# Kernel optimization log

Measured on AMD Instinct MI355X. Metric: run time of the kernel, lower is better.

Reference implementation:

```python
import jax, jax.numpy as jnp
from jax import lax
import numpy as np

BS, C_IN, C_OUT, STYLE_D, H, W, F = 8, 256, 256, 512, 64, 64, 3


def setup_inputs() -> dict:
    key = jax.random.key(0)
    k = jax.random.split(key, 6)
    # xavier_uniform for conv weight: gain=1, fan_in=c_in*f*f, fan_out=c_out*f*f
    fan_in, fan_out = C_IN * F * F, C_OUT * F * F
    limit_w = float(np.sqrt(6.0 / (fan_in + fan_out)))
    limit_a = float(np.sqrt(1.0 / STYLE_D))  # torch Linear default init bound
    return {
        "x": jax.random.normal(k[0], (BS, C_IN, H, W), jnp.float32),
        "s": jax.random.normal(k[1], (BS, STYLE_D), jnp.float32),
        "w": jax.random.uniform(k[2], (C_OUT, C_IN, F, F), jnp.float32, -limit_w, limit_w),
        "b": jnp.zeros((C_OUT, 1, 1), jnp.float32),
        "affine_w": jax.random.uniform(k[3], (C_IN, STYLE_D), jnp.float32, -limit_a, limit_a),
        "affine_b": jax.random.uniform(k[4], (C_IN,), jnp.float32, -limit_a, limit_a),
    }


def reference(x, s, w, b, affine_w, affine_b):
    bs = x.shape[0]
    # style -> per-channel modulation scales: [bs, c_in]
    style = s @ affine_w.T + affine_b
    # modulate: [bs, c_out, c_in, f, f]
    wmod = w[None, :, :, :, :] * (style[:, None, :, None, None] + 1.0)
    # demodulate
    d = jnp.sqrt(jnp.sum(jnp.square(wmod), axis=(2, 3, 4), keepdims=True) + 1e-8)
    wmod = wmod / d
    # grouped conv with groups=bs (per-sample weights)
    xr = x.reshape(1, bs * x.shape[1], x.shape[2], x.shape[3])
    cw = wmod.reshape(bs * wmod.shape[1], wmod.shape[2], wmod.shape[3], wmod.shape[4])
    out = lax.conv_general_dilated(
        xr, cw, window_strides=(1, 1), padding=((1, 1), (1, 1)),
        dimension_numbers=("NCHW", "OIHW", "NCHW"), feature_group_count=bs)
    out = out.reshape(bs, wmod.shape[1], out.shape[2], out.shape[3])
    return out + b  # b broadcasts as [c_out,1,1]
```

## Files before the change

kernel.cpp:

```cpp
#include <hip/hip_runtime.h>
#include <hip/hip_bf16.h>
#include <stdint.h>

#define BS   8
#define CIN  256
#define COUT 256
#define SD   512
#define HH   64
#define WW   64
#define HP   66

typedef __attribute__((ext_vector_type(8))) short short8;
typedef __attribute__((ext_vector_type(4))) float f32x4;

__device__ __forceinline__ unsigned short f2bf(float f) {
    __hip_bfloat16 h = __float2bfloat16(f);
    return *reinterpret_cast<unsigned short*>(&h);
}

typedef __attribute__((address_space(3))) unsigned int lds_u32_t;
typedef const __attribute__((address_space(1))) unsigned int glb_u32_t;

__device__ __forceinline__ void async16(const void* g, void* l) {
    __builtin_amdgcn_global_load_lds((glb_u32_t*)g, (lds_u32_t*)l, 16, 0, 0);
}

__global__ void k_style(const float* __restrict__ s, const float* __restrict__ aw,
                        const float* __restrict__ ab, float* __restrict__ m) {
    int b = blockIdx.x >> 3, chunk = blockIdx.x & 7;
    int tid = threadIdx.x;
    __shared__ float sv[SD];
    for (int d = tid; d < SD; d += 256) sv[d] = s[b * SD + d];
    __syncthreads();
    int il = tid >> 3, p = tid & 7;
    int i = chunk * 32 + il;
    const float4* awr = (const float4*)(aw + (size_t)i * SD + p * 64);
    float acc = 0.f;
#pragma unroll
    for (int d4 = 0; d4 < 16; ++d4) {
        float4 w4 = awr[d4];
        int d0 = p * 64 + d4 * 4;
        acc += w4.x * sv[d0] + w4.y * sv[d0 + 1] + w4.z * sv[d0 + 2] + w4.w * sv[d0 + 3];
    }
    acc += __shfl_xor(acc, 1);
    acc += __shfl_xor(acc, 2);
    acc += __shfl_xor(acc, 4);
    if (p == 0) m[b * CIN + i] = acc + ab[i] + 1.0f;
}

__global__ void k_prep(const float* __restrict__ w, const float* __restrict__ m,
                       const float* __restrict__ x,
                       unsigned short* __restrict__ wb, float* __restrict__ dinv,
                       unsigned short* __restrict__ xp) {
    __shared__ float red[4][8];
    int tid = threadIdx.x;

    if (blockIdx.x < COUT) {
        int o = blockIdx.x, i = tid;
        const float* wp = w + ((size_t)o * CIN + i) * 9;
        float v[9];
        float q = 0.f;
#pragma unroll
        for (int t = 0; t < 9; ++t) { v[t] = wp[t]; q += v[t] * v[t]; }
#pragma unroll
        for (int t = 0; t < 9; ++t)
            wb[((size_t)t * COUT + o) * CIN + i] = f2bf(v[t]);

        float r[8];
#pragma unroll
        for (int b = 0; b < 8; ++b) {
            float mv = m[b * CIN + i];
            r[b] = q * mv * mv;
        }
#pragma unroll
        for (int b = 0; b < 8; ++b) {
            r[b] += __shfl_xor(r[b], 1);
            r[b] += __shfl_xor(r[b], 2);
            r[b] += __shfl_xor(r[b], 4);
            r[b] += __shfl_xor(r[b], 8);
            r[b] += __shfl_xor(r[b], 16);
            r[b] += __shfl_xor(r[b], 32);
        }
        int lane = i & 63, wid = i >> 6;
        if (lane == 0) {
#pragma unroll
            for (int b = 0; b < 8; ++b) red[wid][b] = r[b];
        }
        __syncthreads();
        if (i < 8) {
            float acc = red[0][i] + red[1][i] + red[2][i] + red[3][i];
            dinv[i * COUT + o] = rsqrtf(acc + 1e-8f);
        }
        return;
    }

    int bi = blockIdx.x - COUT;
    int b = bi / HP, yp = bi % HP;
    unsigned short* row = xp + ((size_t)(b * HP + yp)) * HP * CIN;

    if (yp == 0 || yp == HP - 1) {
        uint4 z = {0u, 0u, 0u, 0u};
        uint4* r = (uint4*)row;
        for (int j = tid; j < HP * CIN / 8; j += 256) r[j] = z;
        return;
    }
    int y = yp - 1;

    if (tid < 64) {
        uint4 z = {0u, 0u, 0u, 0u};
        if (tid < 32) ((uint4*)row)[tid] = z;
        else ((uint4*)(row + (size_t)(HP - 1) * CIN))[tid - 32] = z;
    }

#pragma unroll
    for (int it = 0; it < 2; ++it) {
        int u = it * 256 + tid;
        int x0 = (u & 15) * 4;
        int i0 = (u >> 4) * 8;
        float vv[8][4];
        float mv[8];
#pragma unroll
        for (int k = 0; k < 8; ++k) {
            *(float4*)vv[k] = *(const float4*)&x[(((size_t)b * CIN + i0 + k) * HH + y) * WW + x0];
            mv[k] = m[b * CIN + i0 + k];
        }
#pragma unroll
        for (int j = 0; j < 4; ++j) {
            short8 p;
#pragma unroll
            for (int k = 0; k < 8; ++k)
                p[k] = (short)f2bf(vv[k][j] * mv[k]);
            *(short8*)&row[(size_t)(x0 + j + 1) * CIN + i0] = p;
        }
    }
}

__global__ void __launch_bounds__(256, 2)
k_conv(const unsigned short* __restrict__ xp,
       const unsigned short* __restrict__ wb,
       const float* __restrict__ dinv,
       const float* __restrict__ bias,
       float* __restrict__ out) {
    __shared__ unsigned short Ar[3168 * 8];
    __shared__ unsigned short Bs[3 * 512 * 8];

    int bx = blockIdx.x;
    int mt = bx & 127;
    int n0 = (bx >> 7) << 6;
    int m0 = mt << 8;
    int b  = m0 >> 12;
    int y0 = (m0 >> 6) & 63;

    int tid = threadIdx.x;
    int lane = tid & 63, w = tid >> 6;
    int quad = lane >> 4, mrow = lane & 15;

    f32x4 acc[4][4] = {};

    const unsigned short* xb = xp + (size_t)b * HP * HP * CIN;

    auto stageA = [&](int kc) {
        int ch0 = kc * 64;
#pragma unroll
        for (int k = 0; k < 12; ++k) {
            int sA = k * 256 + tid;
            int rowA = sA / 528;
            int rem = sA - rowA * 528;
            int colA = rem >> 3, c4 = rem & 7;
            async16(xb + ((size_t)(y0 + rowA) * HP + colA) * CIN + ch0 + ((c4 ^ (colA & 7)) << 3),
                    &Ar[sA * 8]);
        }
        if (tid < 96) {
            int sA = 3072 + tid;
            int rowA = sA / 528;
            int rem = sA - rowA * 528;
            int colA = rem >> 3, c4 = rem & 7;
            async16(xb + ((size_t)(y0 + rowA) * HP + colA) * CIN + ch0 + ((c4 ^ (colA & 7)) << 3),
                    &Ar[sA * 8]);
        }
    };

    auto stageB = [&](int tt, int kcc, int buf) {
        const unsigned short* bp = wb + ((size_t)tt * COUT + n0) * CIN + kcc * 64;
        unsigned short* dst = Bs + buf * 4096;
#pragma unroll
        for (int k = 0; k < 2; ++k) {
            int sB = k * 256 + tid;
            int rowB = sB >> 3, c4 = sB & 7;
            async16(bp + (size_t)rowB * CIN + ((c4 ^ (rowB & 7)) << 3), dst + sB * 8);
        }
    };

    stageA(0);
    stageB(0, 0, 0);
    stageB(1, 0, 1);
    __syncthreads();

#pragma unroll 1
    for (int kc = 0; kc < 4; ++kc) {
#pragma unroll
        for (int t = 0; t < 9; ++t) {
            if (t < 7) stageB(t + 2, kc, (t + 2) % 3);
            else if (kc < 3) stageB(t - 7, kc + 1, (t + 2) % 3);

            int dy = t / 3, dx = t - dy * 3;
            int arow = w + dy;
            const unsigned short* Bcur = Bs + (t % 3) * 4096;

            short8 af[2][4], bf[2][4];
#pragma unroll
            for (int h = 0; h < 2; ++h)
#pragma unroll
                for (int i = 0; i < 4; ++i) {
                    int col = mrow + i * 16 + dx;
                    int chunk = arow * 528 + col * 8 + ((h * 4 + quad) ^ (col & 7));
                    af[h][i] = *(const short8*)&Ar[chunk * 8];
                }
#pragma unroll
            for (int h = 0; h < 2; ++h)
#pragma unroll
                for (int j = 0; j < 4; ++j) {
                    int rowB = mrow + j * 16;
                    int chunk = rowB * 8 + ((h * 4 + quad) ^ (rowB & 7));
                    bf[h][j] = *(const short8*)&Bcur[chunk * 8];
                }
#pragma unroll
            for (int h = 0; h < 2; ++h)
#pragma unroll
                for (int i = 0; i < 4; ++i)
#pragma unroll
                    for (int j = 0; j < 4; ++j)
                        acc[i][j] = __builtin_amdgcn_mfma_f32_16x16x32_bf16(
                            af[h][i], bf[h][j], acc[i][j], 0, 0, 0);

            __syncthreads();
            if (t == 8 && kc < 3) {
                stageA(kc + 1);
                __syncthreads();
            }
        }
    }

    int y = y0 + w;
#pragma unroll
    for (int j = 0; j < 4; ++j) {
        int o = n0 + mrow + j * 16;
        float dv = dinv[b * COUT + o];
        float bv = bias[o];
#pragma unroll
        for (int i = 0; i < 4; ++i) {
            int xx = i * 16 + quad * 4;
            f32x4 v = acc[i][j] * dv + bv;
            *(f32x4*)(out + (((size_t)(b * COUT + o) * HH + y) * WW + xx)) = v;
        }
    }
}

extern "C" void kernel_launch(void* const* d_in, const int* in_sizes, int n_in,
                              void* d_out, int out_size, void* d_ws, size_t ws_size,
                              hipStream_t stream) {
    const float* x    = (const float*)d_in[0];
    const float* s    = (const float*)d_in[1];
    const float* w    = (const float*)d_in[2];
    const float* bias = (const float*)d_in[3];
    const float* aw   = (const float*)d_in[4];
    const float* ab   = (const float*)d_in[5];
    float* out = (float*)d_out;

    char* ws = (char*)d_ws;
    float* m            = (float*)(ws + 0);
    float* dinv         = (float*)(ws + 8192);
    unsigned short* wb  = (unsigned short*)(ws + 16384);
    unsigned short* xpb = (unsigned short*)(ws + 1196032);

    k_style<<<64, 256, 0, stream>>>(s, aw, ab, m);
    k_prep<<<COUT + BS * HP, 256, 0, stream>>>(w, m, x, wb, dinv, xpb);
    k_conv<<<512, 256, 0, stream>>>(xpb, wb, dinv, bias, out);
}
```

Measured before the change: 135.3 us.

## Use 512-thread conv blocks and stage all nine tap weight tiles per K chunk

Doubles the conv block to 8 waves, with waves split 4x2 over rows and output channels so each wave accumulates a 4x2 MFMA tile instead of 4x4. The rotating three-buffer per-tap weight pipeline is replaced by loading all nine tap weight tiles for a 64-channel chunk at once, which removes the barrier after every tap and leaves only two per chunk. In exchange, loads no longer overlap compute inside a chunk, pairs of waves read the same A fragments from LDS, and shared memory per block rises to about 124 KB. At that size only one block fits per CU, so occupancy likely falls.

```diff
diff --git a/kernel.cpp b/kernel.cpp
--- a/kernel.cpp
+++ b/kernel.cpp
@@ -135,14 +135,14 @@
     }
 }
 
-__global__ void __launch_bounds__(256, 2)
+__global__ void __launch_bounds__(512, 2)
 k_conv(const unsigned short* __restrict__ xp,
        const unsigned short* __restrict__ wb,
        const float* __restrict__ dinv,
        const float* __restrict__ bias,
        float* __restrict__ out) {
     __shared__ unsigned short Ar[3168 * 8];
-    __shared__ unsigned short Bs[3 * 512 * 8];
+    __shared__ unsigned short Bs[4608 * 8];
 
     int bx = blockIdx.x;
     int mt = bx & 127;
@@ -153,17 +153,18 @@
 
     int tid = threadIdx.x;
     int lane = tid & 63, w = tid >> 6;
+    int wm = w >> 1, wn = w & 1;
     int quad = lane >> 4, mrow = lane & 15;
 
-    f32x4 acc[4][4] = {};
+    f32x4 acc[4][2] = {};
 
     const unsigned short* xb = xp + (size_t)b * HP * HP * CIN;
 
     auto stageA = [&](int kc) {
         int ch0 = kc * 64;
 #pragma unroll
-        for (int k = 0; k < 12; ++k) {
-            int sA = k * 256 + tid;
+        for (int k = 0; k < 6; ++k) {
+            int sA = k * 512 + tid;
             int rowA = sA / 528;
             int rem = sA - rowA * 528;
             int colA = rem >> 3, c4 = rem & 7;
@@ -180,34 +181,28 @@
         }
     };
 
-    auto stageB = [&](int tt, int kcc, int buf) {
-        const unsigned short* bp = wb + ((size_t)tt * COUT + n0) * CIN + kcc * 64;
-        unsigned short* dst = Bs + buf * 4096;
-#pragma unroll
-        for (int k = 0; k < 2; ++k) {
-            int sB = k * 256 + tid;
-            int rowB = sB >> 3, c4 = sB & 7;
-            async16(bp + (size_t)rowB * CIN + ((c4 ^ (rowB & 7)) << 3), dst + sB * 8);
+    auto stageBall = [&](int kc) {
+#pragma unroll
+        for (int k = 0; k < 9; ++k) {
+            int rowB = tid >> 3, c4 = tid & 7;
+            async16(wb + ((size_t)k * COUT + n0 + rowB) * CIN + kc * 64 + ((c4 ^ (rowB & 7)) << 3),
+                    &Bs[(k * 512 + tid) * 8]);
         }
     };
-
-    stageA(0);
-    stageB(0, 0, 0);
-    stageB(1, 0, 1);
-    __syncthreads();
 
 #pragma unroll 1
     for (int kc = 0; kc < 4; ++kc) {
+        if (kc) __syncthreads();
+        stageA(kc);
+        stageBall(kc);
+        __syncthreads();
+
 #pragma unroll
         for (int t = 0; t < 9; ++t) {
-            if (t < 7) stageB(t + 2, kc, (t + 2) % 3);
-            else if (kc < 3) stageB(t - 7, kc + 1, (t + 2) % 3);
-
             int dy = t / 3, dx = t - dy * 3;
-            int arow = w + dy;
-            const unsigned short* Bcur = Bs + (t % 3) * 4096;
-
-            short8 af[2][4], bf[2][4];
+            int arow = wm + dy;
+
+            short8 af[2][4], bf[2][2];
 #pragma unroll
             for (int h = 0; h < 2; ++h)
 #pragma unroll
@@ -219,32 +214,26 @@
 #pragma unroll
             for (int h = 0; h < 2; ++h)
 #pragma unroll
-                for (int j = 0; j < 4; ++j) {
-                    int rowB = mrow + j * 16;
-                    int chunk = rowB * 8 + ((h * 4 + quad) ^ (rowB & 7));
-                    bf[h][j] = *(const short8*)&Bcur[chunk * 8];
+                for (int j = 0; j < 2; ++j) {
+                    int rowB = wn * 32 + mrow + j * 16;
+                    int chunk = t * 512 + rowB * 8 + ((h * 4 + quad) ^ (rowB & 7));
+                    bf[h][j] = *(const short8*)&Bs[chunk * 8];
                 }
 #pragma unroll
             for (int h = 0; h < 2; ++h)
 #pragma unroll
                 for (int i = 0; i < 4; ++i)
 #pragma unroll
-                    for (int j = 0; j < 4; ++j)
+                    for (int j = 0; j < 2; ++j)
                         acc[i][j] = __builtin_amdgcn_mfma_f32_16x16x32_bf16(
                             af[h][i], bf[h][j], acc[i][j], 0, 0, 0);
-
-            __syncthreads();
-            if (t == 8 && kc < 3) {
-                stageA(kc + 1);
-                __syncthreads();
-            }
-        }
-    }
-
-    int y = y0 + w;
-#pragma unroll
-    for (int j = 0; j < 4; ++j) {
-        int o = n0 + mrow + j * 16;
+        }
+    }
+
+    int y = y0 + wm;
+#pragma unroll
+    for (int j = 0; j < 2; ++j) {
+        int o = n0 + wn * 32 + mrow + j * 16;
         float dv = dinv[b * COUT + o];
         float bv = bias[o];
 #pragma unroll
@@ -275,5 +264,5 @@
 
     k_style<<<64, 256, 0, stream>>>(s, aw, ab, m);
     k_prep<<<COUT + BS * HP, 256, 0, stream>>>(w, m, x, wb, dinv, xpb);
-    k_conv<<<512, 256, 0, stream>>>(xpb, wb, dinv, bias, out);
-}
+    k_conv<<<512, 512, 0, stream>>>(xpb, wb, dinv, bias, out);
+}
```

Result: slower. 144.7 us (+6.9%).
